# Kernel optimization log

Hardware: AMD Instinct MI355X
Metric: run time of the kernel (lower is better)

## Reference

```python
import jax, jax.numpy as jnp
import numpy as np

HIDDEN = 1024
HEADS = 16
HEAD_DIM = HIDDEN // HEADS  # 64
MLP_HIDDEN = int(HIDDEN * 4.0)  # 4096
B, L = 2, 2048
EPS_LN = 1e-6
EPS_RMS = 1e-6


def setup_inputs() -> dict:
    key = jax.random.key(0)
    ks = jax.random.split(key, 12)
    s = 0.02
    return {
        "x": jax.random.normal(ks[0], (B, L, HIDDEN), jnp.float32),
        "vec": jax.random.normal(ks[1], (B, HIDDEN), jnp.float32),
        "pe": jax.random.normal(ks[2], (1, 1, L, HEAD_DIM // 2, 2, 2), jnp.float32),
        "w_mod": jax.random.normal(ks[3], (HIDDEN, 3 * HIDDEN), jnp.float32) * s,
        "b_mod": jnp.zeros((3 * HIDDEN,), jnp.float32),
        "w1": jax.random.normal(ks[4], (HIDDEN, 3 * HIDDEN + MLP_HIDDEN), jnp.float32) * s,
        "b1": jnp.zeros((3 * HIDDEN + MLP_HIDDEN,), jnp.float32),
        "w_mlp": jax.random.normal(ks[5], (MLP_HIDDEN, HIDDEN), jnp.float32) * s,
        "b_mlp": jnp.zeros((HIDDEN,), jnp.float32),
        "w2": jax.random.normal(ks[6], (2 * HIDDEN, HIDDEN), jnp.float32) * s,
        "b2": jnp.zeros((HIDDEN,), jnp.float32),
        "q_scale": jnp.ones((HEAD_DIM,), jnp.float32),
        "k_scale": jnp.ones((HEAD_DIM,), jnp.float32),
    }


def _layernorm(x, eps=EPS_LN):
    m = jnp.mean(x, axis=-1, keepdims=True)
    v = jnp.mean(jnp.square(x - m), axis=-1, keepdims=True)
    return (x - m) * jax.lax.rsqrt(v + eps)


def _rmsnorm(x, scale, eps=EPS_RMS):
    rrms = jax.lax.rsqrt(jnp.mean(jnp.square(x), axis=-1, keepdims=True) + eps)
    return x * rrms * scale


def _apply_rope(t, pe):
    # t: [B,H,L,D]; pe: [1,1,L,D//2,2,2]
    t_ = t.reshape(*t.shape[:-1], -1, 1, 2)  # [B,H,L,D//2,1,2]
    out = pe[..., 0] * t_[..., 0] + pe[..., 1] * t_[..., 1]  # [B,H,L,D//2,2]
    return out.reshape(t.shape)


def reference(x, vec, pe, w_mod, b_mod, w1, b1, w_mlp, b_mlp, w2, b2, q_scale, k_scale):
    # adaLN modulation: silu(vec) -> Dense(3*dim) -> shift, scale, gate
    mod = (jax.nn.silu(vec) @ w_mod + b_mod)[:, None, :]  # [B,1,3H]
    shift, scale, gate = jnp.split(mod, 3, axis=-1)
    x_mod = (1.0 + scale) * _layernorm(x) + shift
    # fused QKV + MLP projection
    h = x_mod @ w1 + b1  # [B,L,3H+MH]
    qkv, mlp = h[..., : 3 * HIDDEN], h[..., 3 * HIDDEN :]
    qkv = qkv.reshape(x.shape[0], x.shape[1], 3, HEADS, HEAD_DIM)
    qkv = jnp.transpose(qkv, (2, 0, 3, 1, 4))  # [3,B,H,L,D]
    q, k, v = qkv[0], qkv[1], qkv[2]
    # QK-RMSNorm per head-dim
    q = _rmsnorm(q, q_scale)
    k = _rmsnorm(k, k_scale)
    # RoPE
    q = _apply_rope(q, pe)
    k = _apply_rope(k, pe)
    # attention
    scores = jnp.einsum("bhqd,bhkd->bhqk", q, k) * (HEAD_DIM ** -0.5)
    probs = jax.nn.softmax(scores, axis=-1)
    attn = jnp.einsum("bhqk,bhkd->bhqd", probs, v)
    attn = jnp.transpose(attn, (0, 2, 1, 3)).reshape(x.shape[0], x.shape[1], HIDDEN)
    # mlp branch (Dense with tanh activation per source) + fused output proj
    mlp_out = jnp.tanh(mlp @ w_mlp + b_mlp)
    out = jnp.concatenate([attn, mlp_out], axis=-1) @ w2 + b2
    return x + gate * out
```

## Files before the change

### kernel.cpp

```cpp
#include <hip/hip_runtime.h>
#include <stdint.h>


#define HID  1024
#define NH   16
#define HD   64
#define MLP  4096
#define D1   7168
#define DQKV 3072
#define DCAT 2048
#define BB   2
#define LL   2048
#define TOK  4096

typedef __attribute__((ext_vector_type(8))) short    bf16x8;
typedef __attribute__((ext_vector_type(4))) float    f32x4;
typedef __attribute__((ext_vector_type(4))) unsigned int u32x4;

__device__ __forceinline__ float b2f(unsigned short u) {
    unsigned int v = ((unsigned int)u) << 16;
    float f; __builtin_memcpy(&f, &v, 4); return f;
}
__device__ __forceinline__ unsigned short f2b(float f) {
    unsigned int v; __builtin_memcpy(&v, &f, 4);
    unsigned int r = (v + 0x7FFFu + ((v >> 16) & 1u)) >> 16;
    return (unsigned short)r;
}
__device__ __forceinline__ unsigned int pkbf2(float a, float b) {
    unsigned int ua, ub;
    __builtin_memcpy(&ua, &a, 4); __builtin_memcpy(&ub, &b, 4);
    return ((ua + 0x8000u) >> 16) | ((ub + 0x8000u) & 0xFFFF0000u);
}
__device__ __forceinline__ void gl_lds16(const unsigned short* g, unsigned short* l) {
    __builtin_amdgcn_global_load_lds(
        (const __attribute__((address_space(1))) unsigned int*)(g),
        (__attribute__((address_space(3))) unsigned int*)(l), 16, 0, 0);
}

__global__ void k_transpose_cvt(const float* __restrict__ in,
                                unsigned short* __restrict__ out, int R, int C) {
    __shared__ float tile[32][33];
    int bx = blockIdx.x, by = blockIdx.y;
    int tx = threadIdx.x, ty = threadIdx.y;
    #pragma unroll
    for (int i = 0; i < 4; i++) {
        int r = by * 32 + ty + i * 8;
        int c = bx * 32 + tx;
        tile[ty + i * 8][tx] = in[(size_t)r * C + c];
    }
    __syncthreads();
    #pragma unroll
    for (int i = 0; i < 4; i++) {
        int ro = bx * 32 + ty + i * 8;
        int co = by * 32 + tx;
        out[(size_t)ro * R + co] = f2b(tile[tx][ty + i * 8]);
    }
}

__global__ void k_mod(const float* __restrict__ vec,
                      const float* __restrict__ w_mod,
                      const float* __restrict__ b_mod,
                      float* __restrict__ mod) {
    __shared__ float sv[HID];
    __shared__ float red[8][32];
    int b = blockIdx.y, t = threadIdx.x;
    for (int j = t; j < HID; j += 256) {
        float v = vec[b * HID + j];
        sv[j] = v / (1.0f + __expf(-v));
    }
    __syncthreads();
    int n0 = blockIdx.x * 32;
    int on = t & 31, ks = t >> 5;
    float acc = 0.f;
    const float* wp = w_mod + (size_t)(ks * 128) * 3072 + n0 + on;
    #pragma unroll 4
    for (int k = 0; k < 128; k++) acc += sv[ks * 128 + k] * wp[(size_t)k * 3072];
    red[ks][on] = acc;
    __syncthreads();
    if (t < 32) {
        float s = 0.f;
        #pragma unroll
        for (int i = 0; i < 8; i++) s += red[i][t];
        mod[b * 3072 + n0 + t] = s + b_mod[n0 + t];
    }
}

__global__ void k_lnmod(const float* __restrict__ x,
                        const float* __restrict__ mod,
                        unsigned short* __restrict__ xmod) {
    int tok = blockIdx.x;
    int t = threadIdx.x;
    int b = tok >> 11;
    float4 v4 = *(const float4*)(x + (size_t)tok * HID + t * 4);
    float v0 = v4.x, v1 = v4.y, v2 = v4.z, v3 = v4.w;
    float s  = v0 + v1 + v2 + v3;
    float sq = v0*v0 + v1*v1 + v2*v2 + v3*v3;
    for (int off = 1; off < 64; off <<= 1) {
        s  += __shfl_xor(s,  off);
        sq += __shfl_xor(sq, off);
    }
    __shared__ float ls[4], lq[4];
    int w = t >> 6;
    if ((t & 63) == 0) { ls[w] = s; lq[w] = sq; }
    __syncthreads();
    s  = ls[0] + ls[1] + ls[2] + ls[3];
    sq = lq[0] + lq[1] + lq[2] + lq[3];
    float mean = s * (1.0f / HID);
    float var  = sq * (1.0f / HID) - mean * mean;
    float rstd = rsqrtf(var + 1e-6f);
    const float* mb = mod + b * 3072;
    float y[4] = {v0, v1, v2, v3};
    unsigned short r[4];
    #pragma unroll
    for (int j = 0; j < 4; j++) {
        int col = t * 4 + j;
        float nval = (y[j] - mean) * rstd;
        r[j] = f2b((1.0f + mb[1024 + col]) * nval + mb[col]);
    }
    unsigned int o0 = (unsigned int)r[0] | ((unsigned int)r[1] << 16);
    unsigned int o1 = (unsigned int)r[2] | ((unsigned int)r[3] << 16);
    *(uint2*)(xmod + (size_t)tok * HID + t * 4) = make_uint2(o0, o1);
}

template<int EPI>
__global__ __launch_bounds__(256) void k_gemm(
    const unsigned short* __restrict__ A, int lda,
    const unsigned short* __restrict__ Bt, int ldb,
    const float* __restrict__ bias,
    unsigned short* __restrict__ C, float* __restrict__ Cf, int ldc,
    int K,
    const float* __restrict__ xin,
    const float* __restrict__ mod) {
    __shared__ alignas(16) unsigned short As[128 * 32];
    __shared__ alignas(16) unsigned short Bs[128 * 32];
    int t = threadIdx.x;
    int bm = blockIdx.x, bn = blockIdx.y;
    int lane = t & 63, wave = t >> 6;
    int wm = (wave >> 1) * 64, wn = (wave & 1) * 64;
    int ln = lane & 15, kq = lane >> 4;

    f32x4 acc[4][4];
    #pragma unroll
    for (int i = 0; i < 4; i++)
        #pragma unroll
        for (int j = 0; j < 4; j++) acc[i][j] = {0.f, 0.f, 0.f, 0.f};

    int r0 = t >> 2, c0 = (t & 3) * 8;
    const unsigned short* Ab = A  + (size_t)(bm * 128) * lda;
    const unsigned short* Bb = Bt + (size_t)(bn * 128) * ldb;

    for (int k0 = 0; k0 < K; k0 += 32) {
        __syncthreads();
        gl_lds16(Ab + (size_t)r0 * lda + k0 + c0,        &As[t * 8]);
        gl_lds16(Ab + (size_t)(r0 + 64) * lda + k0 + c0, &As[2048 + t * 8]);
        gl_lds16(Bb + (size_t)r0 * ldb + k0 + c0,        &Bs[t * 8]);
        gl_lds16(Bb + (size_t)(r0 + 64) * ldb + k0 + c0, &Bs[2048 + t * 8]);
        __syncthreads();
        bf16x8 af[4], bfr[4];
        #pragma unroll
        for (int i = 0; i < 4; i++)
            af[i] = *(const bf16x8*)(&As[(wm + i * 16 + ln) * 32 + kq * 8]);
        #pragma unroll
        for (int j = 0; j < 4; j++)
            bfr[j] = *(const bf16x8*)(&Bs[(wn + j * 16 + ln) * 32 + kq * 8]);
        #pragma unroll
        for (int i = 0; i < 4; i++)
            #pragma unroll
            for (int j = 0; j < 4; j++)
                acc[i][j] = __builtin_amdgcn_mfma_f32_16x16x32_bf16(af[i], bfr[j], acc[i][j], 0, 0, 0);
    }

    #pragma unroll
    for (int i = 0; i < 4; i++) {
        #pragma unroll
        for (int j = 0; j < 4; j++) {
            int col = bn * 128 + wn + j * 16 + ln;
            float bv = bias[col];
            #pragma unroll
            for (int r = 0; r < 4; r++) {
                int row = bm * 128 + wm + i * 16 + kq * 4 + r;
                float v = acc[i][j][r] + bv;
                if (EPI == 0) {
                    C[(size_t)row * ldc + col] = f2b(v);
                } else if (EPI == 1) {
                    C[(size_t)row * ldc + col] = f2b(tanhf(v));
                } else {
                    int b = row >> 11;
                    Cf[(size_t)row * ldc + col] =
                        xin[(size_t)row * HID + col] + mod[b * 3072 + 2048 + col] * v;
                }
            }
        }
    }
}

__global__ void k_qkrope(unsigned short* __restrict__ h,
                         const float* __restrict__ pe,
                         const float* __restrict__ q_scale,
                         const float* __restrict__ k_scale) {
    int tok = blockIdx.x;
    int l = tok & (LL - 1);
    int t = threadIdx.x;
    int lane = t & 63, wave = t >> 6;
    int hh = wave * 4 + (lane >> 4);
    int d0 = (lane & 15) * 4;
    unsigned short* row = h + (size_t)tok * D1;
    int i0 = d0 >> 1;
    const float* peb = pe + ((size_t)l * 32 + i0) * 4;
    float4 e0 = *(const float4*)(peb);
    float4 e1 = *(const float4*)(peb + 4);
    #pragma unroll
    for (int qk = 0; qk < 2; qk++) {
        unsigned short* p = row + qk * HID + hh * HD + d0;
        const float* sc = (qk == 0 ? q_scale : k_scale) + d0;
        uint2 qv = *(const uint2*)p;
        float v0 = b2f((unsigned short)(qv.x & 0xFFFF)), v1 = b2f((unsigned short)(qv.x >> 16));
        float v2 = b2f((unsigned short)(qv.y & 0xFFFF)), v3 = b2f((unsigned short)(qv.y >> 16));
        float ssq = v0*v0 + v1*v1 + v2*v2 + v3*v3;
        ssq += __shfl_xor(ssq, 1, 16);
        ssq += __shfl_xor(ssq, 2, 16);
        ssq += __shfl_xor(ssq, 4, 16);
        ssq += __shfl_xor(ssq, 8, 16);
        float rr = rsqrtf(ssq * (1.0f / HD) + 1e-6f);
        if (qk == 0) rr *= 0.18033688011112042f;
        v0 *= rr * sc[0];
        v1 *= rr * sc[1];
        v2 *= rr * sc[2];
        v3 *= rr * sc[3];
        float o0 = e0.x*v0 + e0.y*v1;
        float o1 = e0.z*v0 + e0.w*v1;
        float o2 = e1.x*v2 + e1.y*v3;
        float o3 = e1.z*v2 + e1.w*v3;
        *(uint2*)p = make_uint2(pkbf2(o0, o1), pkbf2(o2, o3));
    }
}

#define KT 64
#define LDP 72
__global__ __launch_bounds__(256) void k_attn(const unsigned short* __restrict__ h,
                                              unsigned short* __restrict__ cat) {
    __shared__ unsigned short Ks[KT * LDP];
    __shared__ unsigned short Vt[HD * LDP];
    __shared__ unsigned short Ps[4 * 32 * LDP];
    int t = threadIdx.x;
    int bx = blockIdx.x;
    int bh = blockIdx.y;
    int b = bh >> 4, hh = bh & 15;
    int lane = t & 63, w = t >> 6;
    int ln = lane & 15, quad = lane >> 4;
    const unsigned short* hb = h + (size_t)b * LL * D1;

    bf16x8 qf[2][2];
    {
        const unsigned short* qbase = hb + (size_t)(bx * 128 + w * 32) * D1 + hh * HD;
        #pragma unroll
        for (int qt = 0; qt < 2; qt++)
            #pragma unroll
            for (int ks = 0; ks < 2; ks++)
                qf[qt][ks] = *(const bf16x8*)(qbase + (size_t)(qt * 16 + ln) * D1 + ks * 32 + quad * 8);
    }

    f32x4 O[4][2];
    #pragma unroll
    for (int vn = 0; vn < 4; vn++)
        #pragma unroll
        for (int qt = 0; qt < 2; qt++) O[vn][qt] = {0.f, 0.f, 0.f, 0.f};
    float m_[2] = {-1e30f, -1e30f};
    float l_[2] = {0.f, 0.f};

    unsigned short* Psw = Ps + w * 32 * LDP;

    int skey = t >> 2, sdc = (t & 3) * 16;
    int p2 = (t & 31) * 2, db = (t >> 5) * 8;

    for (int kb = 0; kb < LL / KT; kb++) {
        __syncthreads();
        {
            const unsigned short* kbase = hb + (size_t)(kb * KT) * D1 + HID + hh * HD;
            u32x4 ka = *(const u32x4*)(kbase + (size_t)skey * D1 + sdc);
            u32x4 kc = *(const u32x4*)(kbase + (size_t)skey * D1 + sdc + 8);
            *(u32x4*)(&Ks[skey * LDP + sdc]) = ka;
            *(u32x4*)(&Ks[skey * LDP + sdc + 8]) = kc;
            const unsigned short* vbase = hb + (size_t)(kb * KT) * D1 + 2 * HID + hh * HD;
            u32x4 va = *(const u32x4*)(vbase + (size_t)p2 * D1 + db);
            u32x4 vb = *(const u32x4*)(vbase + (size_t)(p2 + 1) * D1 + db);
            #pragma unroll
            for (int j = 0; j < 8; j++) {
                unsigned int lo = (j & 1) ? (va[j >> 1] >> 16) : (va[j >> 1] & 0xFFFFu);
                unsigned int hi = (j & 1) ? (vb[j >> 1] >> 16) : (vb[j >> 1] & 0xFFFFu);
                *(unsigned int*)(&Vt[(db + j) * LDP + p2]) = lo | (hi << 16);
            }
        }
        __syncthreads();

        f32x4 st[4][2];
        #pragma unroll
        for (int kt = 0; kt < 4; kt++) {
            st[kt][0] = {0.f, 0.f, 0.f, 0.f};
            st[kt][1] = {0.f, 0.f, 0.f, 0.f};
            #pragma unroll
            for (int ks = 0; ks < 2; ks++) {
                bf16x8 kf = *(const bf16x8*)(&Ks[(kt * 16 + ln) * LDP + ks * 32 + quad * 8]);
                st[kt][0] = __builtin_amdgcn_mfma_f32_16x16x32_bf16(kf, qf[0][ks], st[kt][0], 0, 0, 0);
                st[kt][1] = __builtin_amdgcn_mfma_f32_16x16x32_bf16(kf, qf[1][ks], st[kt][1], 0, 0, 0);
            }
        }

        #pragma unroll
        for (int qt = 0; qt < 2; qt++) {
            float p[16];
            float mx = -1e30f;
            #pragma unroll
            for (int kt = 0; kt < 4; kt++)
                #pragma unroll
                for (int r = 0; r < 4; r++) {
                    float v = st[kt][qt][r];
                    p[kt * 4 + r] = v;
                    mx = fmaxf(mx, v);
                }
            mx = fmaxf(mx, __shfl_xor(mx, 16));
            mx = fmaxf(mx, __shfl_xor(mx, 32));
            float mnew = fmaxf(m_[qt], mx);
            float alpha = __builtin_amdgcn_exp2f(m_[qt] - mnew);
            m_[qt] = mnew;
            float sum = 0.f;
            #pragma unroll
            for (int i = 0; i < 16; i++) {
                float e = __builtin_amdgcn_exp2f(p[i] - mnew);
                p[i] = e;
                sum += e;
            }
            sum += __shfl_xor(sum, 16);
            sum += __shfl_xor(sum, 32);
            l_[qt] = l_[qt] * alpha + sum;
            #pragma unroll
            for (int vn = 0; vn < 4; vn++)
                #pragma unroll
                for (int r = 0; r < 4; r++) O[vn][qt][r] *= alpha;
            #pragma unroll
            for (int kt = 0; kt < 4; kt++) {
                unsigned long long pk =
                    (unsigned long long)pkbf2(p[kt*4+0], p[kt*4+1])
                  | ((unsigned long long)pkbf2(p[kt*4+2], p[kt*4+3]) << 32);
                *(unsigned long long*)(&Psw[(qt * 16 + ln) * LDP + kt * 16 + quad * 4]) = pk;
            }
        }

        #pragma unroll
        for (int kt2 = 0; kt2 < 2; kt2++) {
            bf16x8 pb0 = *(const bf16x8*)(&Psw[(0  + ln) * LDP + kt2 * 32 + quad * 8]);
            bf16x8 pb1 = *(const bf16x8*)(&Psw[(16 + ln) * LDP + kt2 * 32 + quad * 8]);
            #pragma unroll
            for (int vn = 0; vn < 4; vn++) {
                bf16x8 vf = *(const bf16x8*)(&Vt[(vn * 16 + ln) * LDP + kt2 * 32 + quad * 8]);
                O[vn][0] = __builtin_amdgcn_mfma_f32_16x16x32_bf16(vf, pb0, O[vn][0], 0, 0, 0);
                O[vn][1] = __builtin_amdgcn_mfma_f32_16x16x32_bf16(vf, pb1, O[vn][1], 0, 0, 0);
            }
        }
    }

    #pragma unroll
    for (int qt = 0; qt < 2; qt++) {
        float rl = 1.0f / l_[qt];
        size_t row = (size_t)(b * LL + bx * 128 + w * 32 + qt * 16 + ln);
        #pragma unroll
        for (int vn = 0; vn < 4; vn++) {
            #pragma unroll
            for (int r2 = 0; r2 < 4; r2 += 2) {
                unsigned int pk = pkbf2(O[vn][qt][r2] * rl, O[vn][qt][r2 + 1] * rl);
                *(unsigned int*)(&cat[row * DCAT + hh * HD + vn * 16 + quad * 4 + r2]) = pk;
            }
        }
    }
}

extern "C" void kernel_launch(void* const* d_in, const int* in_sizes, int n_in,
                              void* d_out, int out_size, void* d_ws, size_t ws_size,
                              hipStream_t stream) {
    const float* x       = (const float*)d_in[0];
    const float* vec     = (const float*)d_in[1];
    const float* pe      = (const float*)d_in[2];
    const float* w_mod   = (const float*)d_in[3];
    const float* b_mod   = (const float*)d_in[4];
    const float* w1      = (const float*)d_in[5];
    const float* b1      = (const float*)d_in[6];
    const float* w_mlp   = (const float*)d_in[7];
    const float* b_mlp   = (const float*)d_in[8];
    const float* w2      = (const float*)d_in[9];
    const float* b2      = (const float*)d_in[10];
    const float* q_scale = (const float*)d_in[11];
    const float* k_scale = (const float*)d_in[12];
    float* out = (float*)d_out;

    char* ws = (char*)d_ws;
    size_t off = 0;
    float* mod = (float*)(ws + off);                     off += 6144 * 4;
    unsigned short* xmod  = (unsigned short*)(ws + off); off += (size_t)TOK * HID * 2;
    unsigned short* h     = (unsigned short*)(ws + off); off += (size_t)TOK * D1 * 2;
    unsigned short* cat   = (unsigned short*)(ws + off); off += (size_t)TOK * DCAT * 2;
    unsigned short* w1T   = (unsigned short*)(ws + off); off += (size_t)D1 * HID * 2;
    unsigned short* wmlpT = (unsigned short*)(ws + off); off += (size_t)HID * MLP * 2;
    unsigned short* w2T   = (unsigned short*)(ws + off); off += (size_t)HID * DCAT * 2;

    k_transpose_cvt<<<dim3(D1 / 32, HID / 32), dim3(32, 8), 0, stream>>>(w1, w1T, HID, D1);
    k_transpose_cvt<<<dim3(HID / 32, MLP / 32), dim3(32, 8), 0, stream>>>(w_mlp, wmlpT, MLP, HID);
    k_transpose_cvt<<<dim3(HID / 32, DCAT / 32), dim3(32, 8), 0, stream>>>(w2, w2T, DCAT, HID);

    k_mod<<<dim3(96, BB), 256, 0, stream>>>(vec, w_mod, b_mod, mod);
    k_lnmod<<<TOK, 256, 0, stream>>>(x, mod, xmod);

    k_gemm<0><<<dim3(TOK / 128, D1 / 128), 256, 0, stream>>>(
        xmod, HID, w1T, HID, b1, h, nullptr, D1, HID, nullptr, nullptr);

    k_qkrope<<<TOK, 256, 0, stream>>>(h, pe, q_scale, k_scale);

    k_attn<<<dim3(LL / 128, BB * NH), 256, 0, stream>>>(h, cat);

    k_gemm<1><<<dim3(TOK / 128, HID / 128), 256, 0, stream>>>(
        h + DQKV, D1, wmlpT, MLP, b_mlp, cat + HID, nullptr, DCAT, MLP, nullptr, nullptr);

    k_gemm<2><<<dim3(TOK / 128, HID / 128), 256, 0, stream>>>(
        cat, DCAT, w2T, DCAT, b2, nullptr, out, HID, DCAT, x, mod);
}
```

Measured before the change: 484.6 us.

## Split-K the MLP and output GEMMs and XOR-swizzle GEMM LDS tiles

Adds an XOR swizzle to the LDS layout of the GEMM tiles so that MFMA fragment reads spread across banks and avoid conflicts. The MLP and output projection GEMMs, which have only 256 blocks each, now use split-K over two z-slices to give the GPU more blocks to work on. Their partial sums go to an fp32 workspace, and separate reduce kernels then apply bias plus tanh, or the gated residual. This costs extra global traffic for the partials and two additional kernel launches.

```diff
diff --git a/kernel.cpp b/kernel.cpp
--- a/kernel.cpp
+++ b/kernel.cpp
@@ -138,6 +138,8 @@
     int lane = t & 63, wave = t >> 6;
     int wm = (wave >> 1) * 64, wn = (wave & 1) * 64;
     int ln = lane & 15, kq = lane >> 4;
+    int cs  = (((t & 3) ^ ((t >> 4) & 3)) * 8);
+    int kqs = (kq ^ ((ln >> 2) & 3)) * 8;
 
     f32x4 acc[4][4];
     #pragma unroll
@@ -145,24 +147,27 @@
         #pragma unroll
         for (int j = 0; j < 4; j++) acc[i][j] = {0.f, 0.f, 0.f, 0.f};
 
-    int r0 = t >> 2, c0 = (t & 3) * 8;
+    int r0 = t >> 2;
     const unsigned short* Ab = A  + (size_t)(bm * 128) * lda;
     const unsigned short* Bb = Bt + (size_t)(bn * 128) * ldb;
 
-    for (int k0 = 0; k0 < K; k0 += 32) {
+    int ksplit = K / gridDim.z;
+    int kbeg = blockIdx.z * ksplit, kend = kbeg + ksplit;
+
+    for (int k0 = kbeg; k0 < kend; k0 += 32) {
         __syncthreads();
-        gl_lds16(Ab + (size_t)r0 * lda + k0 + c0,        &As[t * 8]);
-        gl_lds16(Ab + (size_t)(r0 + 64) * lda + k0 + c0, &As[2048 + t * 8]);
-        gl_lds16(Bb + (size_t)r0 * ldb + k0 + c0,        &Bs[t * 8]);
-        gl_lds16(Bb + (size_t)(r0 + 64) * ldb + k0 + c0, &Bs[2048 + t * 8]);
+        gl_lds16(Ab + (size_t)r0 * lda + k0 + cs,        &As[t * 8]);
+        gl_lds16(Ab + (size_t)(r0 + 64) * lda + k0 + cs, &As[2048 + t * 8]);
+        gl_lds16(Bb + (size_t)r0 * ldb + k0 + cs,        &Bs[t * 8]);
+        gl_lds16(Bb + (size_t)(r0 + 64) * ldb + k0 + cs, &Bs[2048 + t * 8]);
         __syncthreads();
         bf16x8 af[4], bfr[4];
         #pragma unroll
         for (int i = 0; i < 4; i++)
-            af[i] = *(const bf16x8*)(&As[(wm + i * 16 + ln) * 32 + kq * 8]);
+            af[i] = *(const bf16x8*)(&As[(wm + i * 16 + ln) * 32 + kqs]);
         #pragma unroll
         for (int j = 0; j < 4; j++)
-            bfr[j] = *(const bf16x8*)(&Bs[(wn + j * 16 + ln) * 32 + kq * 8]);
+            bfr[j] = *(const bf16x8*)(&Bs[(wn + j * 16 + ln) * 32 + kqs]);
         #pragma unroll
         for (int i = 0; i < 4; i++)
             #pragma unroll
@@ -175,7 +180,7 @@
         #pragma unroll
         for (int j = 0; j < 4; j++) {
             int col = bn * 128 + wn + j * 16 + ln;
-            float bv = bias[col];
+            float bv = (EPI == 3) ? 0.f : bias[col];
             #pragma unroll
             for (int r = 0; r < 4; r++) {
                 int row = bm * 128 + wm + i * 16 + kq * 4 + r;
@@ -184,14 +189,55 @@
                     C[(size_t)row * ldc + col] = f2b(v);
                 } else if (EPI == 1) {
                     C[(size_t)row * ldc + col] = f2b(tanhf(v));
-                } else {
+                } else if (EPI == 2) {
                     int b = row >> 11;
                     Cf[(size_t)row * ldc + col] =
                         xin[(size_t)row * HID + col] + mod[b * 3072 + 2048 + col] * v;
+                } else {
+                    Cf[((size_t)blockIdx.z * TOK + row) * ldc + col] = v;
                 }
             }
         }
     }
+}
+
+__global__ __launch_bounds__(256) void k_red1(const float* __restrict__ part,
+                                              const float* __restrict__ bias,
+                                              unsigned short* __restrict__ cat) {
+    int idx = blockIdx.x * 256 + threadIdx.x;
+    int row = idx >> 8;
+    int c4  = (idx & 255) * 4;
+    float4 p0 = *(const float4*)(part + (size_t)row * HID + c4);
+    float4 p1 = *(const float4*)(part + ((size_t)TOK + row) * HID + c4);
+    float4 bv = *(const float4*)(bias + c4);
+    float a0 = tanhf(p0.x + p1.x + bv.x);
+    float a1 = tanhf(p0.y + p1.y + bv.y);
+    float a2 = tanhf(p0.z + p1.z + bv.z);
+    float a3 = tanhf(p0.w + p1.w + bv.w);
+    *(uint2*)(&cat[(size_t)row * DCAT + HID + c4]) =
+        make_uint2(pkbf2(a0, a1), pkbf2(a2, a3));
+}
+
+__global__ __launch_bounds__(256) void k_red2(const float* __restrict__ part,
+                                              const float* __restrict__ bias,
+                                              const float* __restrict__ x,
+                                              const float* __restrict__ mod,
+                                              float* __restrict__ out) {
+    int idx = blockIdx.x * 256 + threadIdx.x;
+    int row = idx >> 8;
+    int c4  = (idx & 255) * 4;
+    int b = row >> 11;
+    float4 p0 = *(const float4*)(part + (size_t)row * HID + c4);
+    float4 p1 = *(const float4*)(part + ((size_t)TOK + row) * HID + c4);
+    float4 bv = *(const float4*)(bias + c4);
+    float4 gv = *(const float4*)(mod + b * 3072 + 2048 + c4);
+    float4 xv = *(const float4*)(x + (size_t)row * HID + c4);
+    float4 o;
+    o.x = xv.x + gv.x * (p0.x + p1.x + bv.x);
+    o.y = xv.y + gv.y * (p0.y + p1.y + bv.y);
+    o.z = xv.z + gv.z * (p0.z + p1.z + bv.z);
+    o.w = xv.w + gv.w * (p0.w + p1.w + bv.w);
+    *(float4*)(out + (size_t)row * HID + c4) = o;
 }
 
 __global__ void k_qkrope(unsigned short* __restrict__ h,
@@ -401,6 +447,7 @@
     unsigned short* w1T   = (unsigned short*)(ws + off); off += (size_t)D1 * HID * 2;
     unsigned short* wmlpT = (unsigned short*)(ws + off); off += (size_t)HID * MLP * 2;
     unsigned short* w2T   = (unsigned short*)(ws + off); off += (size_t)HID * DCAT * 2;
+    float* part = (float*)(ws + off);                    off += (size_t)2 * TOK * HID * 4;
 
     k_transpose_cvt<<<dim3(D1 / 32, HID / 32), dim3(32, 8), 0, stream>>>(w1, w1T, HID, D1);
     k_transpose_cvt<<<dim3(HID / 32, MLP / 32), dim3(32, 8), 0, stream>>>(w_mlp, wmlpT, MLP, HID);
@@ -416,9 +463,11 @@
 
     k_attn<<<dim3(LL / 128, BB * NH), 256, 0, stream>>>(h, cat);
 
-    k_gemm<1><<<dim3(TOK / 128, HID / 128), 256, 0, stream>>>(
-        h + DQKV, D1, wmlpT, MLP, b_mlp, cat + HID, nullptr, DCAT, MLP, nullptr, nullptr);
-
-    k_gemm<2><<<dim3(TOK / 128, HID / 128), 256, 0, stream>>>(
-        cat, DCAT, w2T, DCAT, b2, nullptr, out, HID, DCAT, x, mod);
-}
+    k_gemm<3><<<dim3(TOK / 128, HID / 128, 2), 256, 0, stream>>>(
+        h + DQKV, D1, wmlpT, MLP, b_mlp, nullptr, part, HID, MLP, nullptr, nullptr);
+    k_red1<<<TOK * HID / 1024, 256, 0, stream>>>(part, b_mlp, cat);
+
+    k_gemm<3><<<dim3(TOK / 128, HID / 128, 2), 256, 0, stream>>>(
+        cat, DCAT, w2T, DCAT, b2, nullptr, part, HID, DCAT, nullptr, nullptr);
+    k_red2<<<TOK * HID / 1024, 256, 0, stream>>>(part, b2, x, mod, out);
+}
```

Measured after the change: 447.3 us. 1.08x faster.
